# Optimization experiments

Measured on AMD Instinct MI355X. Metric: run time of the kernel, lower is better.

## Reference

```python
import jax, jax.numpy as jnp
import numpy as np

N_NODES = 50000
N_EDGES = 400000
H = 128
L = 3
T = 2
FEAT = 4
N_DATA = 40000


def setup_inputs() -> dict:
    key = jax.random.key(0)
    ks = jax.random.split(key, 12)
    s = lambda k, shape, fan: jax.random.normal(k, shape, dtype=jnp.float32) / np.sqrt(fan)
    inp = {
        'x': jax.random.normal(ks[0], (N_NODES, FEAT), dtype=jnp.float32),
        'edge_index': jax.random.randint(ks[1], (2, N_EDGES), 0, N_NODES, dtype=jnp.int64) if jax.config.jax_enable_x64 else jax.random.randint(ks[1], (2, N_EDGES), 0, N_NODES).astype(jnp.int32),
        'edge_type': jax.random.randint(ks[2], (N_EDGES,), 0, T).astype(jnp.int32),
        'n_data': N_DATA,
        'W_in': s(ks[3], (FEAT, H), FEAT),
        'b_in': jnp.zeros((H,), jnp.float32),
        'W1': s(ks[4], (L, T, 2 * H, H), 2 * H),
        'b1': jnp.zeros((L, T, H), jnp.float32),
        'W2': s(ks[5], (L, T, H, H), H),
        'b2': jnp.zeros((L, T, H), jnp.float32),
        'W_ih': s(ks[6], (L, H, 3 * H), H),
        'b_ih': jnp.zeros((L, 3 * H), jnp.float32),
        'W_hh': s(ks[7], (L, H, 3 * H), H),
        'b_hh': jnp.zeros((L, 3 * H), jnp.float32),
        'Wr1': s(ks[8], (H, H), H),
        'br1': jnp.zeros((H,), jnp.float32),
        'Wr2': s(ks[9], (H, 1), H),
        'br2': jnp.zeros((1,), jnp.float32),
    }
    return inp


def _gru_cell(agg, h, W_ih, b_ih, W_hh, b_hh):
    # torch GRUCell: gates ordered (r, z, n)
    gi = agg @ W_ih + b_ih  # [N, 3H]
    gh = h @ W_hh + b_hh    # [N, 3H]
    i_r, i_z, i_n = jnp.split(gi, 3, axis=-1)
    h_r, h_z, h_n = jnp.split(gh, 3, axis=-1)
    r = jax.nn.sigmoid(i_r + h_r)
    z = jax.nn.sigmoid(i_z + h_z)
    n = jnp.tanh(i_n + r * h_n)
    return (1.0 - z) * n + z * h


def reference(x, edge_index, edge_type, n_data, W_in, b_in, W1, b1, W2, b2,
              W_ih, b_ih, W_hh, b_hh, Wr1, br1, Wr2, br2):
    num_nodes = x.shape[0]
    h = jax.nn.relu(x @ W_in + b_in)  # input_proj (dropout = identity in eval)
    src, dst = edge_index[0], edge_index[1]
    n_layers, n_types = W1.shape[0], W1.shape[1]
    for l in range(n_layers):
        cat = jnp.concatenate([h[src], h[dst]], axis=1)  # [E, 2H]
        msgs = jnp.zeros((cat.shape[0], h.shape[1]), dtype=h.dtype)
        for t in range(n_types):
            m_t = jax.nn.relu(cat @ W1[l, t] + b1[l, t]) @ W2[l, t] + b2[l, t]
            msgs = jnp.where((edge_type == t)[:, None], m_t, msgs)
        agg = jax.ops.segment_sum(msgs, dst, num_segments=num_nodes)  # scatter_add
        h = _gru_cell(agg, h, W_ih[l], b_ih[l], W_hh[l], b_hh[l])
    data_emb = h[:n_data]  # node_type==0 nodes are the first n_data nodes
    out = jax.nn.relu(data_emb @ Wr1 + br1) @ Wr2 + br2  # readout
    return out[:, 0]
```

## Files before the change

### kernel.cpp

```cpp
#include <hip/hip_runtime.h>
#include <math.h>


#define H 128
#define TE2 128
#define MS2 132
#define HS  136
#define FEAT 4
#define WG_PER_LAYER 196608

typedef __bf16 bf16x8 __attribute__((ext_vector_type(8)));
typedef __bf16 bf16x4 __attribute__((ext_vector_type(4)));
typedef float  f32x4  __attribute__((ext_vector_type(4)));

__global__ __launch_bounds__(256) void k_input(
    const float* __restrict__ x, const float* __restrict__ Win,
    const float* __restrict__ bin, float* __restrict__ h,
    __bf16* __restrict__ hb, int n_nodes)
{
    int idx = blockIdx.x * 256 + threadIdx.x;
    if (idx >= n_nodes * H) return;
    int n = idx >> 7, j = idx & 127;
    float acc = bin[j];
#pragma unroll
    for (int f = 0; f < FEAT; f++)
        acc += x[n * FEAT + f] * Win[f * H + j];
    float v = fmaxf(acc, 0.f);
    h[idx] = v;
    hb[idx] = (__bf16)v;
}

__global__ __launch_bounds__(256) void k_wconv(
    const float* __restrict__ W1, const float* __restrict__ W2,
    __bf16* __restrict__ Wsw)
{
    int gid = blockIdx.x * 256 + threadIdx.x;
    const int per_lt = 12 * 4096;
    if (gid >= 6 * per_lt) return;
    int lt = gid / per_lt, rem = gid % per_lt;
    int chunk = rem >> 12;
    int within = rem & 4095;
    int ct = within >> 9;
    int lane = (within >> 3) & 63;
    int j = within & 7;
    int r = lane & 15, quad = lane >> 4;
    int n = ct * 16 + r;
    float v;
    if (chunk < 8) {
        int k = chunk * 32 + quad * 8 + j;
        v = W1[((size_t)lt * 256 + k) * 128 + n];
    } else {
        int k = (chunk - 8) * 32 + quad * 8 + j;
        v = W2[((size_t)lt * 128 + k) * 128 + n];
    }
    Wsw[gid] = (__bf16)v;
}

__global__ __launch_bounds__(256) void k_wgconv(
    const float* __restrict__ Wih, const float* __restrict__ Whh,
    __bf16* __restrict__ Wg)
{
    int gid = blockIdx.x * 256 + threadIdx.x;
    if (gid >= 3 * WG_PER_LAYER) return;
    int layer = gid / WG_PER_LAYER, rem = gid % WG_PER_LAYER;
    int t = rem & 7;
    int lane = (rem >> 3) & 63;
    int jtg = (rem >> 9) % 24;
    int mk = rem / 12288;
    int kc = mk & 3;
    int msplit = mk >> 2;
    int mat = msplit >> 1, split = msplit & 1;
    int r = lane & 15, quad = lane >> 4;
    int k = kc * 32 + quad * 8 + t;
    int n = jtg * 16 + r;
    const float* W = (mat ? Whh : Wih) + (size_t)layer * 128 * 384;
    float v = W[(size_t)k * 384 + n];
    __bf16 hi = (__bf16)v;
    Wg[gid] = split ? (__bf16)(v - (float)hi) : hi;
}

__global__ __launch_bounds__(256) void k_hist(
    const int* __restrict__ et, const int* __restrict__ dst,
    int* __restrict__ cnt, int n_edges, int nn)
{
    int i = blockIdx.x * 256 + threadIdx.x;
    if (i < n_edges) atomicAdd(&cnt[et[i] * nn + dst[i]], 1);
}

__global__ __launch_bounds__(1024) void k_scan1(
    const int* __restrict__ cnt, int* __restrict__ bsum, int n)
{
    int i = blockIdx.x * 1024 + threadIdx.x;
    int v = (i < n) ? cnt[i] : 0;
#pragma unroll
    for (int off = 32; off > 0; off >>= 1) v += __shfl_down(v, off, 64);
    __shared__ int ws[16];
    int lane = threadIdx.x & 63, w = threadIdx.x >> 6;
    if (lane == 0) ws[w] = v;
    __syncthreads();
    if (threadIdx.x < 16) {
        int x = ws[threadIdx.x];
#pragma unroll
        for (int off = 8; off > 0; off >>= 1) x += __shfl_down(x, off, 64);
        if (threadIdx.x == 0) bsum[blockIdx.x] = x;
    }
}

__global__ __launch_bounds__(128) void k_scan2(
    int* __restrict__ bsum, int* __restrict__ offs, int nb, int n)
{
    int lane = threadIdx.x & 63, w = threadIdx.x >> 6;
    int v = (threadIdx.x < nb) ? bsum[threadIdx.x] : 0;
    int orig = v;
#pragma unroll
    for (int off = 1; off < 64; off <<= 1) {
        int t = __shfl_up(v, off, 64);
        if (lane >= off) v += t;
    }
    __shared__ int w0sum;
    if (threadIdx.x == 63) w0sum = v;
    __syncthreads();
    int ex = v - orig + (w ? w0sum : 0);
    if (threadIdx.x < nb) bsum[threadIdx.x] = ex;
    if (threadIdx.x == nb - 1) offs[n] = ex + orig;
}

__global__ __launch_bounds__(1024) void k_scan3(
    const int* __restrict__ cnt, const int* __restrict__ bsum,
    int* __restrict__ offs, int n)
{
    int i = blockIdx.x * 1024 + threadIdx.x;
    int v = (i < n) ? cnt[i] : 0;
    int orig = v;
    int lane = threadIdx.x & 63, w = threadIdx.x >> 6;
#pragma unroll
    for (int off = 1; off < 64; off <<= 1) {
        int t = __shfl_up(v, off, 64);
        if (lane >= off) v += t;
    }
    __shared__ int ws[16];
    if (lane == 63) ws[w] = v;
    __syncthreads();
    if (threadIdx.x < 16) {
        int x = ws[threadIdx.x];
#pragma unroll
        for (int off = 1; off < 16; off <<= 1) {
            int t = __shfl_up(x, off, 64);
            if (lane >= off) x += t;
        }
        ws[threadIdx.x] = x;
    }
    __syncthreads();
    int wbase = w ? ws[w - 1] : 0;
    if (i < n) offs[i] = bsum[blockIdx.x] + wbase + v - orig;
}

__global__ __launch_bounds__(256) void k_place(
    const int* __restrict__ et, const int* __restrict__ dst,
    const int* __restrict__ offs, int* __restrict__ cnt,
    int* __restrict__ bucket, int n_edges, int nn)
{
    int i = blockIdx.x * 256 + threadIdx.x;
    if (i < n_edges) {
        int key = et[i] * nn + dst[i];
        int p = atomicAdd(&cnt[key], -1) - 1;
        bucket[offs[key] + p] = i;
    }
}

__global__ __launch_bounds__(512, 4) void k_msg(
    const __bf16* __restrict__ hb,
    const int* __restrict__ bucket, const int* __restrict__ offs,
    const int* __restrict__ src, const int* __restrict__ dst,
    const __bf16* __restrict__ Wsw, const float* __restrict__ b1l,
    const float* __restrict__ b2l,
    float* __restrict__ agg, int n_edges, int nn)
{
    const int t = blockIdx.y;
    const int c0 = offs[nn];
    const int cnt = t ? (n_edges - c0) : c0;
    const int base = t ? c0 : 0;
    const int start = blockIdx.x * TE2;
    if (start >= cnt) return;

    const __bf16* __restrict__ W = Wsw + (size_t)t * 12 * 4096;
    const float*  __restrict__ b1 = b1l + t * H;
    const float*  __restrict__ b2 = b2l + t * H;

    __shared__ __bf16 sW[4096];
    __shared__ float  sMsg[TE2 * MS2];
    __shared__ int    sDstV[TE2];

    const int tid  = threadIdx.x;
    const int lane = tid & 63;
    const int w    = tid >> 6;
    const int r    = lane & 15;
    const int quad = lane >> 4;

    f32x4 wreg[12];
#pragma unroll
    for (int c = 0; c < 12; c++)
        wreg[c] = *(const f32x4*)(W + c * 4096 + tid * 8);

    if (tid < TE2) {
        int i = start + tid;
        sDstV[tid] = (i < cnt) ? dst[bucket[base + i]] : -1;
    }

    int ei = start + w * 16 + r;
    int e = bucket[base + (ei < cnt ? ei : cnt - 1)];
    const __bf16* aps = hb + (size_t)src[e] * H;
    const __bf16* apd = hb + (size_t)dst[e] * H;

    bf16x8 afS[4];
#pragma unroll
    for (int i = 0; i < 4; i++)
        afS[i] = *(const bf16x8*)(aps + i * 32 + quad * 8);

    __syncthreads();

    f32x4 acc[8];
#pragma unroll
    for (int ct = 0; ct < 8; ct++) acc[ct] = (f32x4){0.f, 0.f, 0.f, 0.f};

    bf16x8 afD[4];
#pragma unroll
    for (int kc = 0; kc < 8; kc++) {
        __syncthreads();
        *(f32x4*)(sW + tid * 8) = wreg[kc];
        __syncthreads();
        if (kc == 2) {
#pragma unroll
            for (int i = 0; i < 4; i++)
                afD[i] = *(const bf16x8*)(apd + i * 32 + quad * 8);
        }
        bf16x8 b = (kc < 4) ? afS[kc] : afD[kc - 4];
#pragma unroll
        for (int ct = 0; ct < 8; ct++) {
            bf16x8 a = *(const bf16x8*)(sW + ct * 512 + lane * 8);
            acc[ct] = __builtin_amdgcn_mfma_f32_16x16x32_bf16(a, b, acc[ct], 0, 0, 0);
        }
    }

    __bf16* sHid = (__bf16*)(sMsg + w * 16 * MS2);
#pragma unroll
    for (int ct = 0; ct < 8; ct++) {
        f32x4 bb4 = *(const f32x4*)(b1 + ct * 16 + quad * 4);
        bf16x4 hv;
#pragma unroll
        for (int g = 0; g < 4; g++)
            hv[g] = (__bf16)fmaxf(acc[ct][g] + bb4[g], 0.f);
        *(bf16x4*)(sHid + r * HS + ct * 16 + quad * 4) = hv;
    }

    f32x4 acc2[8];
#pragma unroll
    for (int ct = 0; ct < 8; ct++) acc2[ct] = (f32x4){0.f, 0.f, 0.f, 0.f};
#pragma unroll
    for (int kc = 0; kc < 4; kc++) {
        __syncthreads();
        *(f32x4*)(sW + tid * 8) = wreg[8 + kc];
        __syncthreads();
        bf16x8 b = *(const bf16x8*)(sHid + r * HS + kc * 32 + quad * 8);
#pragma unroll
        for (int ct = 0; ct < 8; ct++) {
            bf16x8 a = *(const bf16x8*)(sW + ct * 512 + lane * 8);
            acc2[ct] = __builtin_amdgcn_mfma_f32_16x16x32_bf16(a, b, acc2[ct], 0, 0, 0);
        }
    }

#pragma unroll
    for (int ct = 0; ct < 8; ct++) {
        f32x4 bb4 = *(const f32x4*)(b2 + ct * 16 + quad * 4);
        f32x4 mv;
#pragma unroll
        for (int g = 0; g < 4; g++)
            mv[g] = acc2[ct][g] + bb4[g];
        *(f32x4*)(sMsg + (w * 16 + r) * MS2 + ct * 16 + quad * 4) = mv;
    }
    __syncthreads();

    {
        int j = tid & 127, strip = tid >> 7;
        int e0 = strip * 32;
        float run = 0.f; int curd = -1;
        for (int q = 0; q < 32; q++) {
            int d = sDstV[e0 + q];
            float v = sMsg[(e0 + q) * MS2 + j];
            if (d != curd) {
                if (curd >= 0) atomicAdd(agg + (size_t)curd * H + j, run);
                run = 0.f; curd = d;
            }
            if (d >= 0) run += v;
        }
        if (curd >= 0) atomicAdd(agg + (size_t)curd * H + j, run);
    }
}

__global__ __launch_bounds__(512, 2) void k_gru(
    float* __restrict__ h, __bf16* __restrict__ hb,
    float* __restrict__ agg,
    const __bf16* __restrict__ Wg,
    const float* __restrict__ bih, const float* __restrict__ bhh,
    int n_nodes)
{
    const int nb = blockIdx.x * 32;
    const int tid = threadIdx.x;
    __shared__ __bf16 sIn[4][32][HS];

#pragma unroll
    for (int v = 0; v < 2; v++) {
        int idx = tid + 512 * v;
        int e = idx >> 5, c4 = (idx & 31) * 4;
        int n = nb + e;
        float4 av = {0.f, 0.f, 0.f, 0.f}, hv = {0.f, 0.f, 0.f, 0.f};
        if (n < n_nodes) {
            av = *(const float4*)(agg + (size_t)n * H + c4);
            hv = *(const float4*)(h + (size_t)n * H + c4);
            float4 z = {0.f, 0.f, 0.f, 0.f};
            *(float4*)(agg + (size_t)n * H + c4) = z;
        }
        bf16x4 ahi, alo, hhi, hlo;
        float af[4] = {av.x, av.y, av.z, av.w};
        float hf[4] = {hv.x, hv.y, hv.z, hv.w};
#pragma unroll
        for (int c = 0; c < 4; c++) {
            __bf16 ah = (__bf16)af[c]; ahi[c] = ah; alo[c] = (__bf16)(af[c] - (float)ah);
            __bf16 hh = (__bf16)hf[c]; hhi[c] = hh; hlo[c] = (__bf16)(hf[c] - (float)hh);
        }
        *(bf16x4*)&sIn[0][e][c4] = ahi;
        *(bf16x4*)&sIn[1][e][c4] = alo;
        *(bf16x4*)&sIn[2][e][c4] = hhi;
        *(bf16x4*)&sIn[3][e][c4] = hlo;
    }
    __syncthreads();

    const int lane = tid & 63, w = tid >> 6;
    const int r = lane & 15, quad = lane >> 4;
    const int jt = w;

    f32x4 acc[2][3][2];
#pragma unroll
    for (int m = 0; m < 2; m++)
#pragma unroll
        for (int g = 0; g < 3; g++)
#pragma unroll
            for (int mat = 0; mat < 2; mat++)
                acc[m][g][mat] = (f32x4){0.f, 0.f, 0.f, 0.f};

    bf16x8 B[2][12];
#pragma unroll
    for (int mat = 0; mat < 2; mat++)
#pragma unroll
    for (int g = 0; g < 3; g++)
#pragma unroll
    for (int sp = 0; sp < 2; sp++)
        B[0][mat * 6 + g * 2 + sp] = *(const bf16x8*)(Wg +
            ((((size_t)(mat * 2 + sp) * 4 + 0) * 24 + (g * 8 + jt)) * 64 + lane) * 8);

#pragma unroll
    for (int kc = 0; kc < 4; kc++) {
        const int cur = kc & 1, nxt = cur ^ 1;
        if (kc < 3) {
#pragma unroll
            for (int mat = 0; mat < 2; mat++)
#pragma unroll
            for (int g = 0; g < 3; g++)
#pragma unroll
            for (int sp = 0; sp < 2; sp++)
                B[nxt][mat * 6 + g * 2 + sp] = *(const bf16x8*)(Wg +
                    ((((size_t)(mat * 2 + sp) * 4 + (kc + 1)) * 24 + (g * 8 + jt)) * 64 + lane) * 8);
        }
        bf16x8 A[2][4];
#pragma unroll
        for (int m = 0; m < 2; m++)
#pragma unroll
            for (int s = 0; s < 4; s++)
                A[m][s] = *(const bf16x8*)&sIn[s][m * 16 + r][kc * 32 + quad * 8];
#pragma unroll
        for (int g = 0; g < 3; g++)
#pragma unroll
        for (int mat = 0; mat < 2; mat++) {
            bf16x8 bhi = B[cur][mat * 6 + g * 2 + 0];
            bf16x8 blo = B[cur][mat * 6 + g * 2 + 1];
            int s = mat * 2;
#pragma unroll
            for (int m = 0; m < 2; m++) {
                acc[m][g][mat] = __builtin_amdgcn_mfma_f32_16x16x32_bf16(
                    A[m][s], bhi, acc[m][g][mat], 0, 0, 0);
                acc[m][g][mat] = __builtin_amdgcn_mfma_f32_16x16x32_bf16(
                    A[m][s], blo, acc[m][g][mat], 0, 0, 0);
                acc[m][g][mat] = __builtin_amdgcn_mfma_f32_16x16x32_bf16(
                    A[m][s + 1], bhi, acc[m][g][mat], 0, 0, 0);
            }
        }
    }

    const int jcol = jt * 16 + r;
    float br_ = bih[jcol], bz_ = bih[128 + jcol], bn_ = bih[256 + jcol];
    float cr = bhh[jcol], cz = bhh[128 + jcol], cn = bhh[256 + jcol];
#pragma unroll
    for (int m = 0; m < 2; m++)
#pragma unroll
    for (int g4 = 0; g4 < 4; g4++) {
        int n = nb + m * 16 + quad * 4 + g4;
        if (n < n_nodes) {
            float ir = acc[m][0][0][g4], hr = acc[m][0][1][g4];
            float iz = acc[m][1][0][g4], hz = acc[m][1][1][g4];
            float in_ = acc[m][2][0][g4], hn = acc[m][2][1][g4];
            float hold = h[(size_t)n * H + jcol];
            float rr = 1.f / (1.f + expf(-(ir + br_ + hr + cr)));
            float zz = 1.f / (1.f + expf(-(iz + bz_ + hz + cz)));
            float nv = tanhf(in_ + bn_ + rr * (hn + cn));
            float out = (1.f - zz) * nv + zz * hold;
            h[(size_t)n * H + jcol] = out;
            hb[(size_t)n * H + jcol] = (__bf16)out;
        }
    }
}

__global__ __launch_bounds__(128) void k_readout(
    const float* __restrict__ h, const float* __restrict__ Wr1,
    const float* __restrict__ br1, const float* __restrict__ Wr2,
    const float* __restrict__ br2, float* __restrict__ out, int n_out)
{
    const int n0 = blockIdx.x * 16;
    const int tid = threadIdx.x;
    __shared__ float sh[16][H];
    __shared__ float sRed[2][16];
    {
#pragma unroll
        for (int v = 0; v < 4; v++) {
            int idx = tid + 128 * v;
            int e = idx >> 5, q = (idx & 31) * 4;
            int n = n0 + e;
            if (n < n_out)
                *(float4*)&sh[e][q] = *(const float4*)(h + (size_t)n * H + q);
        }
    }
    __syncthreads();

    const int j = tid;
    float bb = br1[j];
    float acc[16];
#pragma unroll
    for (int e = 0; e < 16; e++) acc[e] = bb;
    for (int k = 0; k < H; k++) {
        float wv = Wr1[k * H + j];
#pragma unroll
        for (int e = 0; e < 16; e++) acc[e] += sh[e][k] * wv;
    }
    float w2 = Wr2[j];
    int lane = tid & 63, w = tid >> 6;
#pragma unroll
    for (int e = 0; e < 16; e++) {
        float val = fmaxf(acc[e], 0.f) * w2;
#pragma unroll
        for (int off = 32; off > 0; off >>= 1)
            val += __shfl_down(val, off, 64);
        if (lane == 0) sRed[w][e] = val;
    }
    __syncthreads();
    if (tid < 16 && n0 + tid < n_out)
        out[n0 + tid] = sRed[0][tid] + sRed[1][tid] + br2[0];
}

extern "C" void kernel_launch(void* const* d_in, const int* in_sizes, int n_in,
                              void* d_out, int out_size, void* d_ws, size_t ws_size,
                              hipStream_t stream)
{
    const float* x      = (const float*)d_in[0];
    const int*   eidx   = (const int*)d_in[1];
    const int*   etype  = (const int*)d_in[2];
    const float* Win    = (const float*)d_in[4];
    const float* bin    = (const float*)d_in[5];
    const float* W1     = (const float*)d_in[6];
    const float* b1     = (const float*)d_in[7];
    const float* W2     = (const float*)d_in[8];
    const float* b2     = (const float*)d_in[9];
    const float* Wih    = (const float*)d_in[10];
    const float* bih    = (const float*)d_in[11];
    const float* Whh    = (const float*)d_in[12];
    const float* bhh    = (const float*)d_in[13];
    const float* Wr1    = (const float*)d_in[14];
    const float* br1    = (const float*)d_in[15];
    const float* Wr2    = (const float*)d_in[16];
    const float* br2    = (const float*)d_in[17];

    const int n_nodes = in_sizes[0] / FEAT;
    const int n_edges = in_sizes[1] / 2;
    const int L = 3;
    const size_t nh = (size_t)n_nodes * H;

    const int* src = eidx;
    const int* dst = eidx + n_edges;

    float*  h    = (float*)d_ws;
    float*  agg  = h + nh;
    __bf16* hb   = (__bf16*)(agg + nh);
    __bf16* Wsw  = hb + nh;
    __bf16* Wg   = Wsw + 6 * 12 * 4096;
    int* bucket  = (int*)(Wg + 3 * WG_PER_LAYER);
    int* cnt     = bucket + n_edges;
    int* offs    = cnt + 2 * n_nodes;
    int* bsum    = offs + 2 * n_nodes + 1;

    const int nscan = 2 * n_nodes;
    const int nb = (nscan + 1023) / 1024;

    hipMemsetAsync(cnt, 0, (size_t)nscan * sizeof(int), stream);

    k_wconv<<<(6 * 12 * 4096 + 255) / 256, 256, 0, stream>>>(W1, W2, Wsw);
    k_wgconv<<<(3 * WG_PER_LAYER + 255) / 256, 256, 0, stream>>>(Wih, Whh, Wg);
    k_input<<<((int)nh + 255) / 256, 256, 0, stream>>>(x, Win, bin, h, hb, n_nodes);

    const int eb = (n_edges + 255) / 256;
    k_hist <<<eb, 256, 0, stream>>>(etype, dst, cnt, n_edges, n_nodes);
    k_scan1<<<nb, 1024, 0, stream>>>(cnt, bsum, nscan);
    k_scan2<<<1, 128, 0, stream>>>(bsum, offs, nb, nscan);
    k_scan3<<<nb, 1024, 0, stream>>>(cnt, bsum, offs, nscan);
    k_place<<<eb, 256, 0, stream>>>(etype, dst, offs, cnt, bucket, n_edges, n_nodes);

    hipMemsetAsync(agg, 0, nh * sizeof(float), stream);

    const dim3 mgrid((n_edges + TE2 - 1) / TE2, 2);
    for (int l = 0; l < L; l++) {
        k_msg<<<mgrid, 512, 0, stream>>>(
            hb, bucket, offs, src, dst,
            Wsw + (size_t)l * 2 * 12 * 4096,
            b1 + (size_t)l * 2 * H, b2 + (size_t)l * 2 * H,
            agg, n_edges, n_nodes);
        k_gru<<<(n_nodes + 31) / 32, 512, 0, stream>>>(
            h, hb, agg,
            Wg + (size_t)l * WG_PER_LAYER,
            bih + (size_t)l * 384, bhh + (size_t)l * 384,
            n_nodes);
    }

    k_readout<<<(out_size + 15) / 16, 128, 0, stream>>>(
        h, Wr1, br1, Wr2, br2, (float*)d_out, out_size);
}
```

Measured before the change: 609.6 us.

## Enlarge message tile to 256 edges with 2x4 MFMA register blocking

The edge-message kernel now processes 256 edges per block instead of 128. Each wave computes a 64-column by 64-edge sub-tile, so every weight fragment loaded from shared memory feeds four MFMAs instead of one. Node features are read straight from global memory per k-chunk, and weights are streamed with a one-ahead register prefetch instead of keeping all 12 chunks in registers. Blocks are remapped with a strided chunk order across 8 groups, and the scatter-add runs in two 64-column halves so the output tile fits in the reused hidden buffer. This trades more accumulator registers and extra barriers for less LDS traffic per MFMA.

```diff
diff --git a/kernel.cpp b/kernel.cpp
--- a/kernel.cpp
+++ b/kernel.cpp
@@ -3,8 +3,9 @@
 
 
 #define H 128
-#define TE2 128
-#define MS2 132
+#define TE3 256
+#define HS3 136
+#define MS3 68
 #define HS  136
 #define FEAT 4
 #define WG_PER_LAYER 196608
@@ -180,120 +181,160 @@
     const int c0 = offs[nn];
     const int cnt = t ? (n_edges - c0) : c0;
     const int base = t ? c0 : 0;
-    const int start = blockIdx.x * TE2;
-    if (start >= cnt) return;
+
+    const int B = (cnt + TE3 - 1) / TE3;
+    const int cpx = (B + 7) >> 3;
+    int bx = blockIdx.x;
+    if (bx >= 8 * cpx) return;
+    int chunk = (bx & 7) * cpx + (bx >> 3);
+    if (chunk >= B) return;
+    const int start = chunk * TE3;
 
     const __bf16* __restrict__ W = Wsw + (size_t)t * 12 * 4096;
     const float*  __restrict__ b1 = b1l + t * H;
     const float*  __restrict__ b2 = b2l + t * H;
 
     __shared__ __bf16 sW[4096];
-    __shared__ float  sMsg[TE2 * MS2];
-    __shared__ int    sDstV[TE2];
+    __shared__ __bf16 sHid[TE3 * HS3];
+    float* sMsg = (float*)sHid;
+    __shared__ int sSrcN[TE3], sDstN[TE3], sDstV[TE3];
 
     const int tid  = threadIdx.x;
     const int lane = tid & 63;
     const int w    = tid >> 6;
     const int r    = lane & 15;
     const int quad = lane >> 4;
-
-    f32x4 wreg[12];
-#pragma unroll
-    for (int c = 0; c < 12; c++)
-        wreg[c] = *(const f32x4*)(W + c * 4096 + tid * 8);
-
-    if (tid < TE2) {
+    const int f    = w & 1;
+    const int q    = w >> 1;
+
+    f32x4 wnext = *(const f32x4*)(W + tid * 8);
+
+    if (tid < TE3) {
         int i = start + tid;
-        sDstV[tid] = (i < cnt) ? dst[bucket[base + i]] : -1;
-    }
-
-    int ei = start + w * 16 + r;
-    int e = bucket[base + (ei < cnt ? ei : cnt - 1)];
-    const __bf16* aps = hb + (size_t)src[e] * H;
-    const __bf16* apd = hb + (size_t)dst[e] * H;
-
-    bf16x8 afS[4];
-#pragma unroll
-    for (int i = 0; i < 4; i++)
-        afS[i] = *(const bf16x8*)(aps + i * 32 + quad * 8);
-
-    __syncthreads();
-
-    f32x4 acc[8];
-#pragma unroll
-    for (int ct = 0; ct < 8; ct++) acc[ct] = (f32x4){0.f, 0.f, 0.f, 0.f};
-
-    bf16x8 afD[4];
+        int e = bucket[base + (i < cnt ? i : cnt - 1)];
+        sSrcN[tid] = src[e];
+        int d = dst[e];
+        sDstN[tid] = d;
+        sDstV[tid] = (i < cnt) ? d : -1;
+    }
+    __syncthreads();
+
+    const __bf16* ep[4];
+#pragma unroll
+    for (int et = 0; et < 4; et++)
+        ep[et] = hb + (size_t)sSrcN[q * 64 + et * 16 + r] * H;
+
+    f32x4 acc[4][4];
+#pragma unroll
+    for (int c = 0; c < 4; c++)
+#pragma unroll
+        for (int et = 0; et < 4; et++) acc[c][et] = (f32x4){0.f, 0.f, 0.f, 0.f};
+
 #pragma unroll
     for (int kc = 0; kc < 8; kc++) {
         __syncthreads();
-        *(f32x4*)(sW + tid * 8) = wreg[kc];
+        *(f32x4*)(sW + tid * 8) = wnext;
+        wnext = *(const f32x4*)(W + (kc + 1) * 4096 + tid * 8);
         __syncthreads();
-        if (kc == 2) {
-#pragma unroll
-            for (int i = 0; i < 4; i++)
-                afD[i] = *(const bf16x8*)(apd + i * 32 + quad * 8);
-        }
-        bf16x8 b = (kc < 4) ? afS[kc] : afD[kc - 4];
-#pragma unroll
-        for (int ct = 0; ct < 8; ct++) {
-            bf16x8 a = *(const bf16x8*)(sW + ct * 512 + lane * 8);
-            acc[ct] = __builtin_amdgcn_mfma_f32_16x16x32_bf16(a, b, acc[ct], 0, 0, 0);
-        }
-    }
-
-    __bf16* sHid = (__bf16*)(sMsg + w * 16 * MS2);
-#pragma unroll
-    for (int ct = 0; ct < 8; ct++) {
-        f32x4 bb4 = *(const f32x4*)(b1 + ct * 16 + quad * 4);
-        bf16x4 hv;
-#pragma unroll
-        for (int g = 0; g < 4; g++)
-            hv[g] = (__bf16)fmaxf(acc[ct][g] + bb4[g], 0.f);
-        *(bf16x4*)(sHid + r * HS + ct * 16 + quad * 4) = hv;
-    }
-
-    f32x4 acc2[8];
-#pragma unroll
-    for (int ct = 0; ct < 8; ct++) acc2[ct] = (f32x4){0.f, 0.f, 0.f, 0.f};
+        if (kc == 4) {
+#pragma unroll
+            for (int et = 0; et < 4; et++)
+                ep[et] = hb + (size_t)sDstN[q * 64 + et * 16 + r] * H;
+        }
+        const int kk = (kc & 3) * 32 + quad * 8;
+        bf16x8 Bf[4];
+#pragma unroll
+        for (int et = 0; et < 4; et++)
+            Bf[et] = *(const bf16x8*)(ep[et] + kk);
+        bf16x8 Af[4];
+#pragma unroll
+        for (int c = 0; c < 4; c++)
+            Af[c] = *(const bf16x8*)(sW + (4 * f + c) * 512 + lane * 8);
+#pragma unroll
+        for (int c = 0; c < 4; c++)
+#pragma unroll
+            for (int et = 0; et < 4; et++)
+                acc[c][et] = __builtin_amdgcn_mfma_f32_16x16x32_bf16(
+                    Af[c], Bf[et], acc[c][et], 0, 0, 0);
+    }
+
+#pragma unroll
+    for (int c = 0; c < 4; c++) {
+        f32x4 bb4 = *(const f32x4*)(b1 + (4 * f + c) * 16 + quad * 4);
+#pragma unroll
+        for (int et = 0; et < 4; et++) {
+            bf16x4 hv;
+#pragma unroll
+            for (int g = 0; g < 4; g++)
+                hv[g] = (__bf16)fmaxf(acc[c][et][g] + bb4[g], 0.f);
+            *(bf16x4*)(sHid + (q * 64 + et * 16 + r) * HS3
+                       + (4 * f + c) * 16 + quad * 4) = hv;
+        }
+    }
+
+    f32x4 acc2[4][4];
+#pragma unroll
+    for (int c = 0; c < 4; c++)
+#pragma unroll
+        for (int et = 0; et < 4; et++) acc2[c][et] = (f32x4){0.f, 0.f, 0.f, 0.f};
+
 #pragma unroll
     for (int kc = 0; kc < 4; kc++) {
         __syncthreads();
-        *(f32x4*)(sW + tid * 8) = wreg[8 + kc];
+        *(f32x4*)(sW + tid * 8) = wnext;
+        if (kc < 3)
+            wnext = *(const f32x4*)(W + (9 + kc) * 4096 + tid * 8);
         __syncthreads();
-        bf16x8 b = *(const bf16x8*)(sHid + r * HS + kc * 32 + quad * 8);
-#pragma unroll
-        for (int ct = 0; ct < 8; ct++) {
-            bf16x8 a = *(const bf16x8*)(sW + ct * 512 + lane * 8);
-            acc2[ct] = __builtin_amdgcn_mfma_f32_16x16x32_bf16(a, b, acc2[ct], 0, 0, 0);
-        }
-    }
-
-#pragma unroll
-    for (int ct = 0; ct < 8; ct++) {
-        f32x4 bb4 = *(const f32x4*)(b2 + ct * 16 + quad * 4);
-        f32x4 mv;
-#pragma unroll
-        for (int g = 0; g < 4; g++)
-            mv[g] = acc2[ct][g] + bb4[g];
-        *(f32x4*)(sMsg + (w * 16 + r) * MS2 + ct * 16 + quad * 4) = mv;
-    }
-    __syncthreads();
-
-    {
-        int j = tid & 127, strip = tid >> 7;
+        const int kk = kc * 32 + quad * 8;
+        bf16x8 Bf[4];
+#pragma unroll
+        for (int et = 0; et < 4; et++)
+            Bf[et] = *(const bf16x8*)(sHid + (q * 64 + et * 16 + r) * HS3 + kk);
+        bf16x8 Af[4];
+#pragma unroll
+        for (int c = 0; c < 4; c++)
+            Af[c] = *(const bf16x8*)(sW + (4 * f + c) * 512 + lane * 8);
+#pragma unroll
+        for (int c = 0; c < 4; c++)
+#pragma unroll
+            for (int et = 0; et < 4; et++)
+                acc2[c][et] = __builtin_amdgcn_mfma_f32_16x16x32_bf16(
+                    Af[c], Bf[et], acc2[c][et], 0, 0, 0);
+    }
+
+#pragma unroll
+    for (int p = 0; p < 2; p++) {
+        __syncthreads();
+        if (f == p) {
+#pragma unroll
+            for (int c = 0; c < 4; c++) {
+                f32x4 bb4 = *(const f32x4*)(b2 + (4 * f + c) * 16 + quad * 4);
+#pragma unroll
+                for (int et = 0; et < 4; et++) {
+                    f32x4 mv;
+#pragma unroll
+                    for (int g = 0; g < 4; g++)
+                        mv[g] = acc2[c][et][g] + bb4[g];
+                    *(f32x4*)(sMsg + (q * 64 + et * 16 + r) * MS3
+                              + c * 16 + quad * 4) = mv;
+                }
+            }
+        }
+        __syncthreads();
+        int j = tid & 63, strip = tid >> 6;
+        int jcol = p * 64 + j;
         int e0 = strip * 32;
         float run = 0.f; int curd = -1;
-        for (int q = 0; q < 32; q++) {
-            int d = sDstV[e0 + q];
-            float v = sMsg[(e0 + q) * MS2 + j];
+        for (int qq = 0; qq < 32; qq++) {
+            int d = sDstV[e0 + qq];
+            float v = sMsg[(e0 + qq) * MS3 + j];
             if (d != curd) {
-                if (curd >= 0) atomicAdd(agg + (size_t)curd * H + j, run);
+                if (curd >= 0) atomicAdd(agg + (size_t)curd * H + jcol, run);
                 run = 0.f; curd = d;
             }
             if (d >= 0) run += v;
         }
-        if (curd >= 0) atomicAdd(agg + (size_t)curd * H + j, run);
+        if (curd >= 0) atomicAdd(agg + (size_t)curd * H + jcol, run);
     }
 }
 
@@ -432,10 +473,10 @@
 #pragma unroll
         for (int v = 0; v < 4; v++) {
             int idx = tid + 128 * v;
-            int e = idx >> 5, q = (idx & 31) * 4;
+            int e = idx >> 5, qq = (idx & 31) * 4;
             int n = n0 + e;
             if (n < n_out)
-                *(float4*)&sh[e][q] = *(const float4*)(h + (size_t)n * H + q);
+                *(float4*)&sh[e][qq] = *(const float4*)(h + (size_t)n * H + qq);
         }
     }
     __syncthreads();
@@ -523,7 +564,7 @@
 
     hipMemsetAsync(agg, 0, nh * sizeof(float), stream);
 
-    const dim3 mgrid((n_edges + TE2 - 1) / TE2, 2);
+    const dim3 mgrid((n_edges + TE3 - 1) / TE3 + 7, 2);
     for (int l = 0; l < L; l++) {
         k_msg<<<mgrid, 512, 0, stream>>>(
             hb, bucket, offs, src, dst,
```

Measured after the change: 689.5 us. 1.13x slower.

## Retile edge MLP warps as 2x2 grid to halve LDS weight reads

Applied to the files above, without the earlier changes.

Warps in the edge-message kernel now each cover 32 edges and half of the output columns, instead of 16 edges and all columns. Each weight fragment loaded from LDS is reused across two MFMAs, halving LDS reads per MFMA. Weight register staging drops from 12 to 8 registers by loading the second-layer weights during the first GEMM loop, which lowers register pressure. The cost is a second set of gathered src/dst rows held per thread, and a shared hidden buffer across warps that needs an extra barrier.

```diff
diff --git a/kernel.cpp b/kernel.cpp
--- a/kernel.cpp
+++ b/kernel.cpp
@@ -190,16 +190,19 @@
     __shared__ __bf16 sW[4096];
     __shared__ float  sMsg[TE2 * MS2];
     __shared__ int    sDstV[TE2];
+    __bf16* sHid = (__bf16*)sMsg;
 
     const int tid  = threadIdx.x;
     const int lane = tid & 63;
     const int w    = tid >> 6;
     const int r    = lane & 15;
     const int quad = lane >> 4;
-
-    f32x4 wreg[12];
-#pragma unroll
-    for (int c = 0; c < 12; c++)
+    const int f    = w & 1;
+    const int q    = w >> 1;
+
+    f32x4 wreg[8];
+#pragma unroll
+    for (int c = 0; c < 8; c++)
         wreg[c] = *(const f32x4*)(W + c * 4096 + tid * 8);
 
     if (tid < TE2) {
@@ -207,86 +210,127 @@
         sDstV[tid] = (i < cnt) ? dst[bucket[base + i]] : -1;
     }
 
-    int ei = start + w * 16 + r;
-    int e = bucket[base + (ei < cnt ? ei : cnt - 1)];
-    const __bf16* aps = hb + (size_t)src[e] * H;
-    const __bf16* apd = hb + (size_t)dst[e] * H;
-
-    bf16x8 afS[4];
-#pragma unroll
-    for (int i = 0; i < 4; i++)
-        afS[i] = *(const bf16x8*)(aps + i * 32 + quad * 8);
-
-    __syncthreads();
-
-    f32x4 acc[8];
-#pragma unroll
-    for (int ct = 0; ct < 8; ct++) acc[ct] = (f32x4){0.f, 0.f, 0.f, 0.f};
-
-    bf16x8 afD[4];
+    int ei0 = start + q * 32 + r;
+    int ei1 = ei0 + 16;
+    int e0 = bucket[base + (ei0 < cnt ? ei0 : cnt - 1)];
+    int e1 = bucket[base + (ei1 < cnt ? ei1 : cnt - 1)];
+    const __bf16* ap0 = hb + (size_t)src[e0] * H;
+    const __bf16* ap1 = hb + (size_t)src[e1] * H;
+    const __bf16* dp0 = hb + (size_t)dst[e0] * H;
+    const __bf16* dp1 = hb + (size_t)dst[e1] * H;
+
+    bf16x8 afS[2][4];
+#pragma unroll
+    for (int i = 0; i < 4; i++) {
+        afS[0][i] = *(const bf16x8*)(ap0 + i * 32 + quad * 8);
+        afS[1][i] = *(const bf16x8*)(ap1 + i * 32 + quad * 8);
+    }
+
+    __syncthreads();
+
+    f32x4 acc[4][2];
+#pragma unroll
+    for (int c = 0; c < 4; c++)
+#pragma unroll
+        for (int u = 0; u < 2; u++) acc[c][u] = (f32x4){0.f, 0.f, 0.f, 0.f};
+
+    bf16x8 afD[2][4];
 #pragma unroll
     for (int kc = 0; kc < 8; kc++) {
         __syncthreads();
         *(f32x4*)(sW + tid * 8) = wreg[kc];
+        if (kc < 4)
+            wreg[kc] = *(const f32x4*)(W + (8 + kc) * 4096 + tid * 8);
         __syncthreads();
         if (kc == 2) {
 #pragma unroll
-            for (int i = 0; i < 4; i++)
-                afD[i] = *(const bf16x8*)(apd + i * 32 + quad * 8);
-        }
-        bf16x8 b = (kc < 4) ? afS[kc] : afD[kc - 4];
-#pragma unroll
-        for (int ct = 0; ct < 8; ct++) {
-            bf16x8 a = *(const bf16x8*)(sW + ct * 512 + lane * 8);
-            acc[ct] = __builtin_amdgcn_mfma_f32_16x16x32_bf16(a, b, acc[ct], 0, 0, 0);
-        }
-    }
-
-    __bf16* sHid = (__bf16*)(sMsg + w * 16 * MS2);
-#pragma unroll
-    for (int ct = 0; ct < 8; ct++) {
-        f32x4 bb4 = *(const f32x4*)(b1 + ct * 16 + quad * 4);
-        bf16x4 hv;
-#pragma unroll
-        for (int g = 0; g < 4; g++)
-            hv[g] = (__bf16)fmaxf(acc[ct][g] + bb4[g], 0.f);
-        *(bf16x4*)(sHid + r * HS + ct * 16 + quad * 4) = hv;
-    }
-
-    f32x4 acc2[8];
-#pragma unroll
-    for (int ct = 0; ct < 8; ct++) acc2[ct] = (f32x4){0.f, 0.f, 0.f, 0.f};
+            for (int i = 0; i < 4; i++) {
+                afD[0][i] = *(const bf16x8*)(dp0 + i * 32 + quad * 8);
+                afD[1][i] = *(const bf16x8*)(dp1 + i * 32 + quad * 8);
+            }
+        }
+        bf16x8 Bu0 = (kc < 4) ? afS[0][kc] : afD[0][kc - 4];
+        bf16x8 Bu1 = (kc < 4) ? afS[1][kc] : afD[1][kc - 4];
+        bf16x8 Af[4];
+#pragma unroll
+        for (int c = 0; c < 4; c++)
+            Af[c] = *(const bf16x8*)(sW + (4 * f + c) * 512 + lane * 8);
+#pragma unroll
+        for (int c = 0; c < 4; c++) {
+            acc[c][0] = __builtin_amdgcn_mfma_f32_16x16x32_bf16(
+                Af[c], Bu0, acc[c][0], 0, 0, 0);
+            acc[c][1] = __builtin_amdgcn_mfma_f32_16x16x32_bf16(
+                Af[c], Bu1, acc[c][1], 0, 0, 0);
+        }
+    }
+
+#pragma unroll
+    for (int c = 0; c < 4; c++) {
+        f32x4 bb4 = *(const f32x4*)(b1 + (4 * f + c) * 16 + quad * 4);
+#pragma unroll
+        for (int u = 0; u < 2; u++) {
+            bf16x4 hv;
+#pragma unroll
+            for (int g = 0; g < 4; g++)
+                hv[g] = (__bf16)fmaxf(acc[c][u][g] + bb4[g], 0.f);
+            *(bf16x4*)(sHid + (q * 32 + u * 16 + r) * HS
+                       + (4 * f + c) * 16 + quad * 4) = hv;
+        }
+    }
+
+    f32x4 acc2[4][2];
+#pragma unroll
+    for (int c = 0; c < 4; c++)
+#pragma unroll
+        for (int u = 0; u < 2; u++) acc2[c][u] = (f32x4){0.f, 0.f, 0.f, 0.f};
+
 #pragma unroll
     for (int kc = 0; kc < 4; kc++) {
         __syncthreads();
-        *(f32x4*)(sW + tid * 8) = wreg[8 + kc];
+        *(f32x4*)(sW + tid * 8) = wreg[kc];
         __syncthreads();
-        bf16x8 b = *(const bf16x8*)(sHid + r * HS + kc * 32 + quad * 8);
-#pragma unroll
-        for (int ct = 0; ct < 8; ct++) {
-            bf16x8 a = *(const bf16x8*)(sW + ct * 512 + lane * 8);
-            acc2[ct] = __builtin_amdgcn_mfma_f32_16x16x32_bf16(a, b, acc2[ct], 0, 0, 0);
-        }
-    }
-
-#pragma unroll
-    for (int ct = 0; ct < 8; ct++) {
-        f32x4 bb4 = *(const f32x4*)(b2 + ct * 16 + quad * 4);
-        f32x4 mv;
-#pragma unroll
-        for (int g = 0; g < 4; g++)
-            mv[g] = acc2[ct][g] + bb4[g];
-        *(f32x4*)(sMsg + (w * 16 + r) * MS2 + ct * 16 + quad * 4) = mv;
+        bf16x8 Bu[2];
+#pragma unroll
+        for (int u = 0; u < 2; u++)
+            Bu[u] = *(const bf16x8*)(sHid + (q * 32 + u * 16 + r) * HS
+                                     + kc * 32 + quad * 8);
+        bf16x8 Af[4];
+#pragma unroll
+        for (int c = 0; c < 4; c++)
+            Af[c] = *(const bf16x8*)(sW + (4 * f + c) * 512 + lane * 8);
+#pragma unroll
+        for (int c = 0; c < 4; c++) {
+            acc2[c][0] = __builtin_amdgcn_mfma_f32_16x16x32_bf16(
+                Af[c], Bu[0], acc2[c][0], 0, 0, 0);
+            acc2[c][1] = __builtin_amdgcn_mfma_f32_16x16x32_bf16(
+                Af[c], Bu[1], acc2[c][1], 0, 0, 0);
+        }
+    }
+
+    __syncthreads();
+
+#pragma unroll
+    for (int c = 0; c < 4; c++) {
+        f32x4 bb4 = *(const f32x4*)(b2 + (4 * f + c) * 16 + quad * 4);
+#pragma unroll
+        for (int u = 0; u < 2; u++) {
+            f32x4 mv;
+#pragma unroll
+            for (int g = 0; g < 4; g++)
+                mv[g] = acc2[c][u][g] + bb4[g];
+            *(f32x4*)(sMsg + (q * 32 + u * 16 + r) * MS2
+                      + (4 * f + c) * 16 + quad * 4) = mv;
+        }
     }
     __syncthreads();
 
     {
         int j = tid & 127, strip = tid >> 7;
-        int e0 = strip * 32;
+        int e0s = strip * 32;
         float run = 0.f; int curd = -1;
-        for (int q = 0; q < 32; q++) {
-            int d = sDstV[e0 + q];
-            float v = sMsg[(e0 + q) * MS2 + j];
+        for (int qq = 0; qq < 32; qq++) {
+            int d = sDstV[e0s + qq];
+            float v = sMsg[(e0s + qq) * MS2 + j];
             if (d != curd) {
                 if (curd >= 0) atomicAdd(agg + (size_t)curd * H + j, run);
                 run = 0.f; curd = d;
@@ -432,10 +476,10 @@
 #pragma unroll
         for (int v = 0; v < 4; v++) {
             int idx = tid + 128 * v;
-            int e = idx >> 5, q = (idx & 31) * 4;
+            int e = idx >> 5, qq = (idx & 31) * 4;
             int n = n0 + e;
             if (n < n_out)
-                *(float4*)&sh[e][q] = *(const float4*)(h + (size_t)n * H + q);
+                *(float4*)&sh[e][qq] = *(const float4*)(h + (size_t)n * H + qq);
         }
     }
     __syncthreads();
```

New measurement: 624.1 us. +2.4%, slower.

## Shrink k_msg LDS by splitting message reduction into two column halves

Applied to the files above, without the earlier changes.

The fp32 message staging buffer (128x132 floats) is replaced by a shared bf16 buffer sized 128x136, which holds the hidden activations and then fp32 messages in two 64-column passes. Each pass writes half the columns, syncs, and runs the segmented atomic reduction, which roughly halves LDS per block. Launch bounds rise from 4 to 6 blocks per CU to use the freed LDS for occupancy. The cost is extra barriers, shorter reduction runs (16 edges per strip instead of 32) that may issue more atomics, and tighter register limits that could cause spills.

```diff
diff --git a/kernel.cpp b/kernel.cpp
--- a/kernel.cpp
+++ b/kernel.cpp
@@ -4,7 +4,7 @@
 
 #define H 128
 #define TE2 128
-#define MS2 132
+#define MSH 68
 #define HS  136
 #define FEAT 4
 #define WG_PER_LAYER 196608
@@ -168,7 +168,7 @@
     }
 }
 
-__global__ __launch_bounds__(512, 4) void k_msg(
+__global__ __launch_bounds__(512, 6) void k_msg(
     const __bf16* __restrict__ hb,
     const int* __restrict__ bucket, const int* __restrict__ offs,
     const int* __restrict__ src, const int* __restrict__ dst,
@@ -188,8 +188,10 @@
     const float*  __restrict__ b2 = b2l + t * H;
 
     __shared__ __bf16 sW[4096];
-    __shared__ float  sMsg[TE2 * MS2];
+    __shared__ __bf16 sBuf[TE2 * HS];
     __shared__ int    sDstV[TE2];
+    __bf16* sHid = sBuf;
+    float*  sMsg = (float*)sBuf;
 
     const int tid  = threadIdx.x;
     const int lane = tid & 63;
@@ -242,7 +244,6 @@
         }
     }
 
-    __bf16* sHid = (__bf16*)(sMsg + w * 16 * MS2);
 #pragma unroll
     for (int ct = 0; ct < 8; ct++) {
         f32x4 bb4 = *(const f32x4*)(b1 + ct * 16 + quad * 4);
@@ -250,7 +251,7 @@
 #pragma unroll
         for (int g = 0; g < 4; g++)
             hv[g] = (__bf16)fmaxf(acc[ct][g] + bb4[g], 0.f);
-        *(bf16x4*)(sHid + r * HS + ct * 16 + quad * 4) = hv;
+        *(bf16x4*)(sHid + (w * 16 + r) * HS + ct * 16 + quad * 4) = hv;
     }
 
     f32x4 acc2[8];
@@ -261,7 +262,7 @@
         __syncthreads();
         *(f32x4*)(sW + tid * 8) = wreg[8 + kc];
         __syncthreads();
-        bf16x8 b = *(const bf16x8*)(sHid + r * HS + kc * 32 + quad * 8);
+        bf16x8 b = *(const bf16x8*)(sHid + (w * 16 + r) * HS + kc * 32 + quad * 8);
 #pragma unroll
         for (int ct = 0; ct < 8; ct++) {
             bf16x8 a = *(const bf16x8*)(sW + ct * 512 + lane * 8);
@@ -270,30 +271,35 @@
     }
 
 #pragma unroll
-    for (int ct = 0; ct < 8; ct++) {
-        f32x4 bb4 = *(const f32x4*)(b2 + ct * 16 + quad * 4);
-        f32x4 mv;
-#pragma unroll
-        for (int g = 0; g < 4; g++)
-            mv[g] = acc2[ct][g] + bb4[g];
-        *(f32x4*)(sMsg + (w * 16 + r) * MS2 + ct * 16 + quad * 4) = mv;
-    }
-    __syncthreads();
-
-    {
-        int j = tid & 127, strip = tid >> 7;
-        int e0 = strip * 32;
-        float run = 0.f; int curd = -1;
-        for (int q = 0; q < 32; q++) {
-            int d = sDstV[e0 + q];
-            float v = sMsg[(e0 + q) * MS2 + j];
-            if (d != curd) {
-                if (curd >= 0) atomicAdd(agg + (size_t)curd * H + j, run);
-                run = 0.f; curd = d;
+    for (int p = 0; p < 2; p++) {
+#pragma unroll
+        for (int c = 0; c < 4; c++) {
+            int ct = p * 4 + c;
+            f32x4 bb4 = *(const f32x4*)(b2 + ct * 16 + quad * 4);
+            f32x4 mv;
+#pragma unroll
+            for (int g = 0; g < 4; g++)
+                mv[g] = acc2[ct][g] + bb4[g];
+            *(f32x4*)(sMsg + (w * 16 + r) * MSH + c * 16 + quad * 4) = mv;
+        }
+        __syncthreads();
+        {
+            int j = tid & 63, strip = tid >> 6;
+            int jcol = p * 64 + j;
+            int e0 = strip * 16;
+            float run = 0.f; int curd = -1;
+            for (int qq = 0; qq < 16; qq++) {
+                int d = sDstV[e0 + qq];
+                float v = sMsg[(e0 + qq) * MSH + j];
+                if (d != curd) {
+                    if (curd >= 0) atomicAdd(agg + (size_t)curd * H + jcol, run);
+                    run = 0.f; curd = d;
+                }
+                if (d >= 0) run += v;
             }
-            if (d >= 0) run += v;
-        }
-        if (curd >= 0) atomicAdd(agg + (size_t)curd * H + j, run);
+            if (curd >= 0) atomicAdd(agg + (size_t)curd * H + jcol, run);
+        }
+        __syncthreads();
     }
 }
 
@@ -432,10 +438,10 @@
 #pragma unroll
         for (int v = 0; v < 4; v++) {
             int idx = tid + 128 * v;
-            int e = idx >> 5, q = (idx & 31) * 4;
+            int e = idx >> 5, qq = (idx & 31) * 4;
             int n = n0 + e;
             if (n < n_out)
-                *(float4*)&sh[e][q] = *(const float4*)(h + (size_t)n * H + q);
+                *(float4*)&sh[e][qq] = *(const float4*)(h + (size_t)n * H + qq);
         }
     }
     __syncthreads();
```

Result: slower. 698.8 us (+14.6%).
